# Performance work log

Measured on AMD Instinct MI355X. Metric: run time of the kernel, lower is better.

## Reference

```python
import jax, jax.numpy as jnp
import numpy as np

DAMPENING = 0.3          # dampening_factor
REC_DAMPENING = 0.4      # recurrent_dampening_factor
DT = 1.0
MAX_DELAY = 5
N_BASIS = 5


@jax.custom_vjp
def spike_function(v_scaled):
    # hard threshold with triangular pseudo-derivative (custom gradient)
    return (v_scaled > 0.0).astype(v_scaled.dtype)

def _spike_fwd(v_scaled):
    return spike_function(v_scaled), v_scaled

def _spike_bwd(v_scaled, g):
    return (g * DAMPENING * jnp.maximum(1.0 - jnp.abs(v_scaled), 0.0),)

spike_function.defvjp(_spike_fwd, _spike_bwd)


def setup_inputs() -> dict:
    key = jax.random.key(0)
    ks = jax.random.split(key, 12)
    N, E, T, B = 50000, 2_000_000, 40, 1
    D, n5 = MAX_DELAY, N * N_BASIS
    inp = {}
    inp['weights'] = jax.random.normal(ks[0], (E,), jnp.float32) * 0.01
    inp['edge_basis'] = jax.random.uniform(ks[1], (E, N_BASIS), jnp.float32)
    inp['ext_input'] = jax.random.normal(ks[2], (B, T, n5), jnp.float32) * 0.02
    inp['decay'] = 0.9 + 0.09 * jax.random.uniform(ks[3], (N,), jnp.float32)
    inp['current_factor'] = jax.random.uniform(ks[4], (N,), jnp.float32)
    inp['gathered_g'] = jax.random.normal(ks[5], (N,), jnp.float32) * 0.01
    inp['v_th'] = jnp.ones((N,), jnp.float32)          # normalized threshold
    inp['v_reset'] = jnp.zeros((N,), jnp.float32)
    inp['normalizer'] = jnp.ones((N,), jnp.float32)    # v_th - e_l
    inp['t_ref'] = 2.0 * jnp.ones((N,), jnp.float32)
    inp['exp_dt_k'] = 0.8 + 0.19 * jax.random.uniform(ks[6], (N, 2), jnp.float32)
    inp['asc_amps'] = jax.random.normal(ks[7], (N, 2), jnp.float32) * 0.01
    inp['syn_decay'] = jax.random.uniform(ks[8], (n5,), jnp.float32)
    inp['psc_initial'] = jax.random.uniform(ks[9], (n5,), jnp.float32)
    inp['pre_idx'] = jax.random.randint(ks[10], (E,), 0, D * N, jnp.int32)
    inp['post_idx'] = jax.random.randint(ks[11], (E,), 0, N, jnp.int32)
    return inp


def reference(weights, edge_basis, ext_input, decay, current_factor, gathered_g,
              v_th, v_reset, normalizer, t_ref, exp_dt_k, asc_amps,
              syn_decay, psc_initial, pre_idx, post_idx):
    B, T, n5 = ext_input.shape
    N = n5 // N_BASIS
    D = MAX_DELAY
    # per-edge weight across the 5 synaptic basis filters: [E,5]
    ew = weights[:, None] * edge_basis

    def rec_input(z_flat):  # z_flat: [B, D*N] delayed spike buffer (flattened)
        zg = jnp.take(z_flat, pre_idx, axis=1)                # [B,E] gather presynaptic spikes
        contrib = zg[:, :, None] * ew[None]                    # [B,E,5]
        out = jax.vmap(lambda c: jax.ops.segment_sum(c, post_idx, num_segments=N))(contrib)
        return out.reshape(B, N * N_BASIS)                     # [B,N*5]

    def step(carry, x_t):
        v, r, asc, psc, z_buf = carry
        # recurrent dampening: scale gradient through recurrent spikes
        zd = z_buf * REC_DAMPENING
        zb = jax.lax.stop_gradient(z_buf - zd) + zd
        i_rec = rec_input(zb.reshape(B, D * N))
        new_psc = psc * syn_decay + (i_rec + x_t) * psc_initial      # [B,N*5]
        input_current = new_psc.reshape(B, N, N_BASIS).sum(-1)       # [B,N]
        prev_z = z_buf[:, 0]                                         # most recent spikes
        new_asc = exp_dt_k * asc + prev_z[:, :, None] * asc_amps     # [B,N,2]
        c1 = input_current + new_asc.sum(-1) + gathered_g
        new_v = decay * v + current_factor * c1
        new_v = jnp.where(prev_z > 0.5, v_reset, new_v)              # hard reset
        v_sc = (new_v - v_th) / normalizer
        z = spike_function(v_sc)
        z = jnp.where(r > 0.0, jnp.zeros_like(z), z)                 # refractory block
        new_r = jnp.maximum(r + z * t_ref - DT, 0.0)
        new_buf = jnp.concatenate([z[:, None], z_buf[:, :-1]], axis=1)
        return (new_v, new_r, new_asc, new_psc, new_buf), z

    v0 = jnp.broadcast_to(v_reset, (B, N)).astype(jnp.float32)
    r0 = jnp.zeros((B, N), jnp.float32)
    asc0 = jnp.zeros((B, N, 2), jnp.float32)
    psc0 = jnp.zeros((B, n5), jnp.float32)
    buf0 = jnp.zeros((B, D, N), jnp.float32)
    x_seq = jnp.transpose(ext_input, (1, 0, 2))  # [T,B,N*5]
    _, z_seq = jax.lax.scan(step, (v0, r0, asc0, psc0, buf0), x_seq)
    return jnp.transpose(z_seq, (1, 0, 2))  # [B,T,N] spikes
```

## Files before the change

kernel.cpp:

```cpp
#include <hip/hip_runtime.h>

#define NB_ 5
#define MD_ 5
#define CSL 128
#define CAP 6144
#define CH  4096
#define RING 6


__global__ __launch_bounds__(256) void init_kernel(
    const float* __restrict__ decay, const float* __restrict__ cf,
    const float* __restrict__ g,     const float* __restrict__ vth,
    const float* __restrict__ vrst,  const float* __restrict__ nrm,
    const float* __restrict__ tref,  const float* __restrict__ ek,
    const float* __restrict__ am,
    float4* __restrict__ pk, float* __restrict__ v, int N)
{
    int n = blockIdx.x * blockDim.x + threadIdx.x;
    if (n >= N) return;
    pk[3 * n]     = make_float4(decay[n], cf[n], g[n], vth[n]);
    pk[3 * n + 1] = make_float4(vrst[n], nrm[n], tref[n], ek[2 * n]);
    pk[3 * n + 2] = make_float4(ek[2 * n + 1], am[2 * n], am[2 * n + 1], 0.0f);
    v[n] = vrst[n];
}

__global__ __launch_bounds__(256) void partition_kernel(
    const int* __restrict__ pre_idx,
    int* __restrict__ gcur,
    unsigned* __restrict__ part,
    int E, int N)
{
    __shared__ int cntL[512];
    __shared__ int posL[512];
    int t = threadIdx.x;
    cntL[t] = 0; cntL[t + 256] = 0;
    __syncthreads();
    int e0 = blockIdx.x * CH;
    int e1 = min(e0 + CH, E);
    for (int e = e0 + t; e < e1; e += 256) {
        int pre = pre_idx[e];
        int d = pre / N;
        int n = pre - d * N;
        atomicAdd(&cntL[n >> 7], 1);
    }
    __syncthreads();
    for (int b = t; b < 512; b += 256)
        posL[b] = cntL[b] ? atomicAdd(&gcur[b], cntL[b]) : 0;
    __syncthreads();
    for (int e = e0 + t; e < e1; e += 256) {
        int pre = pre_idx[e];
        int d = pre / N;
        int n = pre - d * N;
        int b = n >> 7;
        int p = atomicAdd(&posL[b], 1);
        if (p < CAP)
            part[(size_t)b * CAP + p] =
                ((unsigned)(n & (CSL - 1)) << 24) | ((unsigned)d << 21) | (unsigned)e;
    }
}

__global__ __launch_bounds__(256) void bucket_sort_kernel(
    const int* __restrict__ gcur,
    const unsigned* __restrict__ part,
    unsigned* __restrict__ edgeRec,
    uint2* __restrict__ rp,
    int N)
{
    __shared__ int h[CSL];
    __shared__ int sc_[CSL];
    __shared__ int pos_[CSL];
    int c = blockIdx.x, t = threadIdx.x;
    int cnt = min(gcur[c], CAP);
    size_t base = (size_t)c * CAP;
    if (t < CSL) h[t] = 0;
    __syncthreads();
    for (int i = t; i < cnt; i += 256)
        atomicAdd(&h[part[base + i] >> 24], 1);
    __syncthreads();
    if (t < CSL) sc_[t] = h[t];
    __syncthreads();
    for (int off = 1; off < CSL; off <<= 1) {
        int y = 0;
        if (t < CSL && t >= off) y = sc_[t - off];
        __syncthreads();
        if (t < CSL && t >= off) sc_[t] += y;
        __syncthreads();
    }
    if (t < CSL) {
        int end = sc_[t];
        pos_[t] = (int)base + end - h[t];
        int gn = c * CSL + t;
        if (gn < N)
            rp[gn] = make_uint2((unsigned)(base + end - h[t]),
                                (unsigned)(base + end));
    }
    __syncthreads();
    for (int i = t; i < cnt; i += 256) {
        unsigned q = part[base + i];
        int dst = atomicAdd(&pos_[q >> 24], 1);
        edgeRec[dst] = q;
    }
}


__global__ __launch_bounds__(256) void step_kernel(
    const float* __restrict__ x_t,
    float*       __restrict__ psc,
    const float* __restrict__ sd,
    const float* __restrict__ pi,
    const float4* __restrict__ pk,
    float* __restrict__ v,
    float* __restrict__ r,
    float* __restrict__ asc,
    float* __restrict__ ring,
    const int* __restrict__ scnt,
    int*       __restrict__ scnt_new,
    const float* __restrict__ out_prev,
    float*       __restrict__ out_t,
    const uint2*    __restrict__ rp,
    const unsigned* __restrict__ edgeRec,
    const float*    __restrict__ weights,
    const float*    __restrict__ edge_basis,
    const int*      __restrict__ post_idx,
    int t, int n5, int N)
{
    __shared__ int   nf_s;
    __shared__ uint2 rowsL[256];
    __shared__ int   scL[256];
    __shared__ int   pref[257];

    const int tloc = threadIdx.x;
    const int n = blockIdx.x * blockDim.x + tloc;
    const bool has = (n < N);
    if (tloc == 0) nf_s = 0;
    __syncthreads();

    const int* sw = scnt + t;
    int scw = sw[0] + sw[1] + sw[2] + sw[3] + sw[4];

    float z = 0.0f;
    if (has) {
        float ir0 = 0.f, ir1 = 0.f, ir2 = 0.f, ir3 = 0.f, ir4 = 0.f;
        float* rg = ring + (size_t)(t % RING) * n5 + (size_t)n * NB_;
        if (scw > 0) {
            ir0 = rg[0]; ir1 = rg[1]; ir2 = rg[2]; ir3 = rg[3]; ir4 = rg[4];
            rg[0] = 0.f; rg[1] = 0.f; rg[2] = 0.f; rg[3] = 0.f; rg[4] = 0.f;
        }

        const float* xp  = x_t + (size_t)n * NB_;
        float*       pp  = psc + (size_t)n * NB_;
        const float* sdp = sd  + (size_t)n * NB_;
        const float* pip = pi  + (size_t)n * NB_;
        float ic = 0.0f, pv;
        pv = pp[0] * sdp[0] + (ir0 + xp[0]) * pip[0]; pp[0] = pv; ic += pv;
        pv = pp[1] * sdp[1] + (ir1 + xp[1]) * pip[1]; pp[1] = pv; ic += pv;
        pv = pp[2] * sdp[2] + (ir2 + xp[2]) * pip[2]; pp[2] = pv; ic += pv;
        pv = pp[3] * sdp[3] + (ir3 + xp[3]) * pip[3]; pp[3] = pv; ic += pv;
        pv = pp[4] * sdp[4] + (ir4 + xp[4]) * pip[4]; pp[4] = pv; ic += pv;

        float4 P0 = pk[3 * n], P1 = pk[3 * n + 1], P2 = pk[3 * n + 2];

        float pz = (t > 0) ? out_prev[n] : 0.0f;

        float a0 = P1.w * asc[2 * n]     + pz * P2.y;
        float a1 = P2.x * asc[2 * n + 1] + pz * P2.z;
        asc[2 * n]     = a0;
        asc[2 * n + 1] = a1;

        float c1 = ic + (a0 + a1) + P0.z;
        float nv = P0.x * v[n] + P0.y * c1;
        if (pz > 0.5f) nv = P1.x;

        float vsc = (nv - P0.w) / P1.y;
        z = (vsc > 0.0f) ? 1.0f : 0.0f;
        float rr = r[n];
        if (rr > 0.0f) z = 0.0f;

        r[n] = fmaxf(rr + z * P1.z - 1.0f, 0.0f);
        v[n] = nv;
        out_t[n] = z;

        if (z != 0.0f) {
            int idx = atomicAdd(&nf_s, 1);
            rowsL[idx] = rp[n];
        }
    }

    unsigned long long m = __ballot(z != 0.0f);
    if ((tloc & 63) == 0 && m)
        atomicAdd(scnt_new, (int)__popcll(m));

    __syncthreads();
    int nf = nf_s;
    if (nf == 0) return;

    int cnt = (tloc < nf) ? (int)(rowsL[tloc].y - rowsL[tloc].x) : 0;
    scL[tloc] = cnt;
    __syncthreads();
    int x = cnt;
    for (int off = 1; off < 256; off <<= 1) {
        int y = (tloc >= off) ? scL[tloc - off] : 0;
        __syncthreads();
        x += y;
        scL[tloc] = x;
        __syncthreads();
    }
    pref[tloc + 1] = scL[tloc];
    if (tloc == 0) pref[0] = 0;
    __syncthreads();

    int tot = pref[nf];
    for (int j = tloc; j < tot; j += 256) {
        int lo = 0, hi = nf - 1;
        while (lo < hi) {
            int mid = (lo + hi + 1) >> 1;
            if (pref[mid] <= j) lo = mid; else hi = mid - 1;
        }
        int i = (int)rowsL[lo].x + (j - pref[lo]);
        unsigned q = edgeRec[i];
        int d = (int)((q >> 21) & 7u);
        int e = (int)(q & 0x1FFFFFu);
        float w = weights[e];
        const float* bs = edge_basis + (size_t)e * NB_;
        float* dst = ring + (size_t)((t + 1 + d) % RING) * n5
                   + (size_t)post_idx[e] * NB_;
        atomicAdd(dst + 0, w * bs[0]);
        atomicAdd(dst + 1, w * bs[1]);
        atomicAdd(dst + 2, w * bs[2]);
        atomicAdd(dst + 3, w * bs[3]);
        atomicAdd(dst + 4, w * bs[4]);
    }
}


extern "C" void kernel_launch(void* const* d_in, const int* in_sizes, int n_in,
                              void* d_out, int out_size, void* d_ws, size_t ws_size,
                              hipStream_t stream)
{
    const float* weights        = (const float*)d_in[0];
    const float* edge_basis     = (const float*)d_in[1];
    const float* ext_input      = (const float*)d_in[2];
    const float* decay          = (const float*)d_in[3];
    const float* current_factor = (const float*)d_in[4];
    const float* gathered_g     = (const float*)d_in[5];
    const float* v_th           = (const float*)d_in[6];
    const float* v_reset        = (const float*)d_in[7];
    const float* normalizer     = (const float*)d_in[8];
    const float* t_ref          = (const float*)d_in[9];
    const float* exp_dt_k       = (const float*)d_in[10];
    const float* asc_amps       = (const float*)d_in[11];
    const float* syn_decay      = (const float*)d_in[12];
    const float* psc_initial    = (const float*)d_in[13];
    const int*   pre_idx        = (const int*)d_in[14];
    const int*   post_idx       = (const int*)d_in[15];

    const int E  = in_sizes[0];
    const int N  = in_sizes[3];
    const int n5 = N * NB_;
    const int T  = in_sizes[2] / n5;

    const int NC = (N + CSL - 1) / CSL;

    float* out = (float*)d_out;

    char* wsb = (char*)d_ws;
    size_t o = 0;
    int*   gcur = (int*)(wsb + o);   o += 512 * 4;
    int*   scnt = (int*)(wsb + o);   o += (size_t)(T + MD_) * 4;
    o = (o + 15) & ~(size_t)15;
    float* psc  = (float*)(wsb + o); o += (size_t)n5 * 4;
    float* r    = (float*)(wsb + o); o += (size_t)N * 4;
    float* asc  = (float*)(wsb + o); o += (size_t)2 * N * 4;
    o = (o + 15) & ~(size_t)15;
    float* ring = (float*)(wsb + o); o += (size_t)RING * n5 * 4;
    size_t zero_bytes = o;
    float*  v       = (float*)(wsb + o);  o += (size_t)N * 4;
    float4* pk      = (float4*)(wsb + o); o += (size_t)N * 12 * 4;
    uint2*  rp      = (uint2*)(wsb + o);  o += (size_t)N * 8;
    o = (o + 15) & ~(size_t)15;
    unsigned* part    = (unsigned*)(wsb + o); o += (size_t)NC * CAP * 4;
    unsigned* edgeRec = (unsigned*)(wsb + o); o += (size_t)NC * CAP * 4;

    hipMemsetAsync(d_ws, 0, zero_bytes, stream);

    init_kernel<<<(N + 255) / 256, 256, 0, stream>>>(
        decay, current_factor, gathered_g, v_th, v_reset, normalizer, t_ref,
        exp_dt_k, asc_amps, pk, v, N);

    const int nbe = (E + CH - 1) / CH;
    partition_kernel<<<nbe, 256, 0, stream>>>(pre_idx, gcur, part, E, N);
    bucket_sort_kernel<<<NC, 256, 0, stream>>>(gcur, part, edgeRec, rp, N);

    const int nblk = (N + 255) / 256;
    for (int t = 0; t < T; ++t) {
        step_kernel<<<nblk, 256, 0, stream>>>(
            ext_input + (size_t)t * n5,
            psc, syn_decay, psc_initial,
            pk, v, r, asc,
            ring, scnt, scnt + MD_ + t,
            out + (size_t)(t > 0 ? t - 1 : 0) * N,
            out + (size_t)t * N,
            rp, edgeRec, weights, edge_basis, post_idx,
            t, n5, N);
    }
}
```

Baseline: 270.4 us.

## Locally sort edge partitions in shared memory and fold init into bucket sort

The partition kernel now handles 8192 edges per block and sorts them by bucket in shared memory using a block-wide scan. It then writes each bucket's run contiguously to global memory, so stores to the partition array are coalesced instead of scattered per edge. The separate init kernel is removed and its per-neuron parameter packing is folded into the bucket sort kernel, saving one launch. The cost is more shared memory per block and fewer partition blocks, which may lower occupancy.

```diff
diff --git a/kernel.cpp b/kernel.cpp
--- a/kernel.cpp
+++ b/kernel.cpp
@@ -4,25 +4,9 @@
 #define MD_ 5
 #define CSL 128
 #define CAP 6144
-#define CH  4096
+#define CH2 8192
 #define RING 6
 
-
-__global__ __launch_bounds__(256) void init_kernel(
-    const float* __restrict__ decay, const float* __restrict__ cf,
-    const float* __restrict__ g,     const float* __restrict__ vth,
-    const float* __restrict__ vrst,  const float* __restrict__ nrm,
-    const float* __restrict__ tref,  const float* __restrict__ ek,
-    const float* __restrict__ am,
-    float4* __restrict__ pk, float* __restrict__ v, int N)
-{
-    int n = blockIdx.x * blockDim.x + threadIdx.x;
-    if (n >= N) return;
-    pk[3 * n]     = make_float4(decay[n], cf[n], g[n], vth[n]);
-    pk[3 * n + 1] = make_float4(vrst[n], nrm[n], tref[n], ek[2 * n]);
-    pk[3 * n + 2] = make_float4(ek[2 * n + 1], am[2 * n], am[2 * n + 1], 0.0f);
-    v[n] = vrst[n];
-}
 
 __global__ __launch_bounds__(256) void partition_kernel(
     const int* __restrict__ pre_idx,
@@ -30,32 +14,64 @@
     unsigned* __restrict__ part,
     int E, int N)
 {
-    __shared__ int cntL[512];
-    __shared__ int posL[512];
-    int t = threadIdx.x;
-    cntL[t] = 0; cntL[t + 256] = 0;
-    __syncthreads();
-    int e0 = blockIdx.x * CH;
-    int e1 = min(e0 + CH, E);
-    for (int e = e0 + t; e < e1; e += 256) {
-        int pre = pre_idx[e];
+    __shared__ unsigned srt[CH2];
+    __shared__ unsigned short bkt[CH2];
+    __shared__ int hist[512];
+    __shared__ int lbase[512];
+    __shared__ int pos[512];
+    __shared__ int gbase[512];
+    __shared__ int tmp[256];
+
+    const int t  = threadIdx.x;
+    const int e0 = blockIdx.x * CH2;
+    const int cnt = min(CH2, E - e0);
+
+    hist[t] = 0; hist[t + 256] = 0;
+    __syncthreads();
+
+    for (int i = t; i < cnt; i += 256) {
+        int pre = pre_idx[e0 + i];
         int d = pre / N;
         int n = pre - d * N;
-        atomicAdd(&cntL[n >> 7], 1);
-    }
-    __syncthreads();
-    for (int b = t; b < 512; b += 256)
-        posL[b] = cntL[b] ? atomicAdd(&gcur[b], cntL[b]) : 0;
-    __syncthreads();
-    for (int e = e0 + t; e < e1; e += 256) {
-        int pre = pre_idx[e];
+        atomicAdd(&hist[n >> 7], 1);
+    }
+    __syncthreads();
+
+    int a = hist[2 * t], b = hist[2 * t + 1], s = a + b;
+    tmp[t] = s;
+    __syncthreads();
+    int x = s;
+    for (int off = 1; off < 256; off <<= 1) {
+        int y = (t >= off) ? tmp[t - off] : 0;
+        __syncthreads();
+        x += y;
+        tmp[t] = x;
+        __syncthreads();
+    }
+    int ep = x - s;
+    lbase[2 * t] = ep;         pos[2 * t] = ep;
+    lbase[2 * t + 1] = ep + a; pos[2 * t + 1] = ep + a;
+    gbase[2 * t]     = a ? atomicAdd(&gcur[2 * t], a) : 0;
+    gbase[2 * t + 1] = b ? atomicAdd(&gcur[2 * t + 1], b) : 0;
+    __syncthreads();
+
+    for (int i = t; i < cnt; i += 256) {
+        int pre = pre_idx[e0 + i];
         int d = pre / N;
         int n = pre - d * N;
-        int b = n >> 7;
-        int p = atomicAdd(&posL[b], 1);
-        if (p < CAP)
-            part[(size_t)b * CAP + p] =
-                ((unsigned)(n & (CSL - 1)) << 24) | ((unsigned)d << 21) | (unsigned)e;
+        int bk = n >> 7;
+        int p = atomicAdd(&pos[bk], 1);
+        srt[p] = ((unsigned)(n & (CSL - 1)) << 24) | ((unsigned)d << 21)
+               | (unsigned)(e0 + i);
+        bkt[p] = (unsigned short)bk;
+    }
+    __syncthreads();
+
+    for (int j = t; j < cnt; j += 256) {
+        int bk = bkt[j];
+        int off2 = gbase[bk] + (j - lbase[bk]);
+        if (off2 < CAP)
+            part[(size_t)bk * CAP + off2] = srt[j];
     }
 }
 
@@ -64,12 +80,29 @@
     const unsigned* __restrict__ part,
     unsigned* __restrict__ edgeRec,
     uint2* __restrict__ rp,
+    const float* __restrict__ decay, const float* __restrict__ cf,
+    const float* __restrict__ g,     const float* __restrict__ vth,
+    const float* __restrict__ vrst,  const float* __restrict__ nrm,
+    const float* __restrict__ tref,  const float* __restrict__ ek,
+    const float* __restrict__ am,
+    float4* __restrict__ pk, float* __restrict__ v,
     int N)
 {
     __shared__ int h[CSL];
     __shared__ int sc_[CSL];
     __shared__ int pos_[CSL];
     int c = blockIdx.x, t = threadIdx.x;
+
+    if (t < CSL) {
+        int n = c * CSL + t;
+        if (n < N) {
+            pk[3 * n]     = make_float4(decay[n], cf[n], g[n], vth[n]);
+            pk[3 * n + 1] = make_float4(vrst[n], nrm[n], tref[n], ek[2 * n]);
+            pk[3 * n + 2] = make_float4(ek[2 * n + 1], am[2 * n], am[2 * n + 1], 0.0f);
+            v[n] = vrst[n];
+        }
+    }
+
     int cnt = min(gcur[c], CAP);
     size_t base = (size_t)c * CAP;
     if (t < CSL) h[t] = 0;
@@ -283,13 +316,12 @@
 
     hipMemsetAsync(d_ws, 0, zero_bytes, stream);
 
-    init_kernel<<<(N + 255) / 256, 256, 0, stream>>>(
+    const int nbe = (E + CH2 - 1) / CH2;
+    partition_kernel<<<nbe, 256, 0, stream>>>(pre_idx, gcur, part, E, N);
+    bucket_sort_kernel<<<NC, 256, 0, stream>>>(
+        gcur, part, edgeRec, rp,
         decay, current_factor, gathered_g, v_th, v_reset, normalizer, t_ref,
         exp_dt_k, asc_amps, pk, v, N);
-
-    const int nbe = (E + CH - 1) / CH;
-    partition_kernel<<<nbe, 256, 0, stream>>>(pre_idx, gcur, part, E, N);
-    bucket_sort_kernel<<<NC, 256, 0, stream>>>(gcur, part, edgeRec, rp, N);
 
     const int nblk = (N + 255) / 256;
     for (int t = 0; t < T; ++t) {
```

After: 275.2 us. Within noise of the previous version (+1.8%).
